# Optimization experiments

Measured on AMD Instinct MI355X. Metric: run time of the kernel, lower is better.

The kernel has to match this reference:

```python
import jax, jax.numpy as jnp
import numpy as np

K = 16  # neighbors per node

def setup_inputs() -> dict:
    key = jax.random.key(0)
    feature = jax.random.normal(key, (16384, 512), dtype=jnp.float32)
    return {"feature": feature, "k": K}

def reference(feature, k):
    # cosine-normalize rows (eps added to norm, matching torch)
    nrm = jnp.linalg.norm(feature, axis=-1, keepdims=True)
    fn = feature / (nrm + 1e-10)
    sim = fn @ fn.T                      # [N, N]
    n = sim.shape[0]
    # zero the diagonal (sim - diag_embed(diag(sim)))
    sim = sim - jnp.diag(jnp.diag(sim))
    _, idx = jax.lax.top_k(sim, k)       # [N, k]
    row = jnp.repeat(jnp.arange(n), k)   # [N*k]
    col = idx.reshape(-1)
    edge_index = jnp.stack([row, col], axis=0).astype(jnp.int64)
    return edge_index
```

## Files before the change

kernel.cpp:

```cpp
#include <hip/hip_runtime.h>
#include <hip/hip_fp16.h>
#include <math.h>

#define NN   16384
#define DD   512
#define KNN  16
#define CAND 24
#define STRIPW 4096
#define NSTRIP (NN / STRIPW)

typedef __attribute__((ext_vector_type(8))) short bf16x8;
typedef __attribute__((ext_vector_type(4))) float f32x4;
typedef unsigned int u32;

__device__ __forceinline__ void load16_lds(const ushort* g, void* l) {
    __builtin_amdgcn_global_load_lds(
        (const __attribute__((address_space(1))) u32*)(const void*)g,
        (__attribute__((address_space(3))) u32*)l, 16, 0, 0);
}

__global__ __launch_bounds__(256) void norm_kernel(const float* __restrict__ feat,
                                                   float* __restrict__ nrm) {
#pragma clang fp contract(off)
    const int t   = threadIdx.x;
    const int row = blockIdx.x * 64 + (t >> 2);
    const int bid = t & 3;
    const float4* p4 = (const float4*)(feat + (size_t)row * DD + bid * 128);
    float r[4][4];
    #pragma unroll
    for (int m = 0; m < 4; m++) {
        float4 q = p4[m];
        r[m][0] = q.x * q.x; r[m][1] = q.y * q.y;
        r[m][2] = q.z * q.z; r[m][3] = q.w * q.w;
    }
    #pragma unroll
    for (int tt = 1; tt < 8; tt++) {
        #pragma unroll
        for (int m = 0; m < 4; m++) {
            float4 q = p4[tt * 4 + m];
            r[m][0] += q.x * q.x; r[m][1] += q.y * q.y;
            r[m][2] += q.z * q.z; r[m][3] += q.w * q.w;
        }
    }
    float v0 = (r[0][0] + r[1][0]) + (r[2][0] + r[3][0]);
    float v1 = (r[0][1] + r[1][1]) + (r[2][1] + r[3][1]);
    float v2 = (r[0][2] + r[1][2]) + (r[2][2] + r[3][2]);
    float v3 = (r[0][3] + r[1][3]) + (r[2][3] + r[3][3]);
    float B  = (v0 + v1) + (v2 + v3);
    B += __shfl_xor(B, 1, 64);
    B += __shfl_xor(B, 2, 64);
    if (bid == 0) nrm[row] = sqrtf(B) + 1e-10f;
}

__device__ inline ushort bf16rne(float f) {
    unsigned u = __float_as_uint(f);
    u += 0x7fffu + ((u >> 16) & 1u);
    return (ushort)(u >> 16);
}
__global__ __launch_bounds__(256) void fn_kernel(const float* __restrict__ feat,
                                                 const float* __restrict__ nrm,
                                                 float* __restrict__ fn,
                                                 ushort* __restrict__ fnb) {
    int i4  = blockIdx.x * 256 + threadIdx.x;
    int row = i4 >> 7;
    float n = nrm[row];
    float4 v = ((const float4*)feat)[i4];
    float4 o = make_float4(v.x / n, v.y / n, v.z / n, v.w / n);
    ((float4*)fn)[i4] = o;
    ushort4 b = {bf16rne(o.x), bf16rne(o.y), bf16rne(o.z), bf16rne(o.w)};
    ((ushort4*)fnb)[i4] = b;
}

__global__ __launch_bounds__(256) void gemm_kernel(const ushort* __restrict__ fnb,
                                                   int stripBase,
                                                   __half* __restrict__ simS) {
    __shared__ ushort As[128 * 64];
    __shared__ ushort Bs[128 * 64];
    const int t    = threadIdx.x;
    const int wave = t >> 6, lane = t & 63;
    const int rbase = blockIdx.y * 128;
    const int cbL   = blockIdx.x * 128;
    const int wr = (wave >> 1) * 64, wc = (wave & 1) * 64;
    const int m = lane & 15, quad = lane >> 4;
    const int rseg = lane >> 3;
    const int cchk = (lane & 7) ^ rseg;

    f32x4 acc[4][4];
    #pragma unroll
    for (int i = 0; i < 4; i++)
        #pragma unroll
        for (int j = 0; j < 4; j++) acc[i][j] = (f32x4){0.f, 0.f, 0.f, 0.f};

    const int swz = ((m & 7) << 4);

    for (int kb = 0; kb < DD; kb += 64) {
        __syncthreads();
        #pragma unroll
        for (int q = 0; q < 4; q++) {
            int s   = wave * 4 + q;
            int row = s * 8 + rseg;
            const ushort* ga = fnb + (size_t)(rbase + row) * DD + kb + cchk * 8;
            const ushort* gb = fnb + (size_t)(stripBase + cbL + row) * DD + kb + cchk * 8;
            load16_lds(ga, (char*)As + s * 1024);
            load16_lds(gb, (char*)Bs + s * 1024);
        }
        __syncthreads();

        #pragma unroll
        for (int ks = 0; ks < 64; ks += 32) {
            const int cb16 = (ks >> 3) + quad;
            const int off  = ((cb16 << 4) ^ swz);
            bf16x8 af[4], bv[4];
            #pragma unroll
            for (int i = 0; i < 4; i++)
                af[i] = *(const bf16x8*)((const char*)As + (wr + i * 16 + m) * 128 + off);
            #pragma unroll
            for (int j = 0; j < 4; j++)
                bv[j] = *(const bf16x8*)((const char*)Bs + (wc + j * 16 + m) * 128 + off);
            #pragma unroll
            for (int i = 0; i < 4; i++)
                #pragma unroll
                for (int j = 0; j < 4; j++)
                    acc[i][j] = __builtin_amdgcn_mfma_f32_16x16x32_bf16(
                        af[i], bv[j], acc[i][j], 0, 0, 0);
        }
    }
    #pragma unroll
    for (int i = 0; i < 4; i++)
        #pragma unroll
        for (int j = 0; j < 4; j++)
            #pragma unroll
            for (int r = 0; r < 4; r++) {
                int grow = rbase + wr + i * 16 + quad * 4 + r;
                int gcol = cbL + wc + j * 16 + m;
                simS[(size_t)grow * STRIPW + gcol] = __float2half(acc[i][j][r]);
            }
}

__global__ __launch_bounds__(256) void select_kernel(const __half2* __restrict__ simS2,
                                                     int stripBase, int firstStrip,
                                                     float* __restrict__ lval,
                                                     int* __restrict__ lidx) {
    const int lane = threadIdx.x & 63;
    const int row  = blockIdx.x * 4 + (threadIdx.x >> 6);
    float lv; int li;
    if (firstStrip) { lv = -3.4e38f; li = 0x7fffffff; }
    else {
        lv = (lane < CAND) ? lval[(size_t)row * CAND + lane] : -3.4e38f;
        li = (lane < CAND) ? lidx[(size_t)row * CAND + lane] : 0x7fffffff;
    }
    const __half2* sp = simS2 + (size_t)row * (STRIPW / 2);
    for (int it = 0; it < STRIPW / 128; it++) {
        __half2 h = sp[it * 64 + lane];
        float v0 = __low2float(h), v1 = __high2float(h);
        int c0 = stripBase + it * 128 + lane * 2, c1 = c0 + 1;
        float vmin = __shfl(lv, CAND - 1);
        int   imin = __shfl(li, CAND - 1);
        bool a0 = ((v0 > vmin) || (v0 == vmin && c0 < imin)) && (c0 != row);
        bool a1 = ((v1 > vmin) || (v1 == vmin && c1 < imin)) && (c1 != row);
        unsigned long long m0 = __ballot(a0), m1 = __ballot(a1);
        #pragma unroll
        for (int ph = 0; ph < 2; ph++) {
            unsigned long long mask = ph ? m1 : m0;
            float vv = ph ? v1 : v0;
            while (mask) {
                int src = __builtin_ctzll(mask); mask &= mask - 1;
                float bvv = __shfl(vv, src);
                int   bc  = stripBase + it * 128 + src * 2 + ph;
                bool better = (lv > bvv) || (lv == bvv && li < bc);
                unsigned long long bb = __ballot(better) & ((1ull << CAND) - 1);
                int p = __popcll(bb);
                if (p < CAND) {
                    float pv = __shfl_up(lv, 1);
                    int   pi = __shfl_up(li, 1);
                    float nlv = (lane < p) ? lv : (lane == p ? bvv : pv);
                    int   nli = (lane < p) ? li : (lane == p ? bc : pi);
                    if (lane < CAND) { lv = nlv; li = nli; }
                }
            }
        }
    }
    if (lane < CAND) {
        lval[(size_t)row * CAND + lane] = lv;
        lidx[(size_t)row * CAND + lane] = li;
    }
}

__global__ __launch_bounds__(256) void rescore_kernel(const float* __restrict__ fn,
                                                      const int* __restrict__ lidx,
                                                      int* __restrict__ out) {
    __shared__ float sv[8][CAND];
    __shared__ int   si[8][CAND];
    const int w    = threadIdx.x >> 5;
    const int lane = threadIdx.x & 31;
    const int row  = blockIdx.x * 8 + w;
    const bool valid = lane < CAND;
    const int c = valid ? lidx[(size_t)row * CAND + lane] : 0;
    const float* q = fn + (size_t)row * DD;
    const float* p = fn + (size_t)c * DD;
    float s = 0.0f;
    for (int k = 0; k < DD; k += 16) {
        float4 q0 = *(const float4*)(q + k),      p0 = *(const float4*)(p + k);
        float4 q1 = *(const float4*)(q + k + 4),  p1 = *(const float4*)(p + k + 4);
        float4 q2 = *(const float4*)(q + k + 8),  p2 = *(const float4*)(p + k + 8);
        float4 q3 = *(const float4*)(q + k + 12), p3 = *(const float4*)(p + k + 12);
        s = __builtin_fmaf(q0.x, p0.x, s); s = __builtin_fmaf(q0.y, p0.y, s);
        s = __builtin_fmaf(q0.z, p0.z, s); s = __builtin_fmaf(q0.w, p0.w, s);
        s = __builtin_fmaf(q1.x, p1.x, s); s = __builtin_fmaf(q1.y, p1.y, s);
        s = __builtin_fmaf(q1.z, p1.z, s); s = __builtin_fmaf(q1.w, p1.w, s);
        s = __builtin_fmaf(q2.x, p2.x, s); s = __builtin_fmaf(q2.y, p2.y, s);
        s = __builtin_fmaf(q2.z, p2.z, s); s = __builtin_fmaf(q2.w, p2.w, s);
        s = __builtin_fmaf(q3.x, p3.x, s); s = __builtin_fmaf(q3.y, p3.y, s);
        s = __builtin_fmaf(q3.z, p3.z, s); s = __builtin_fmaf(q3.w, p3.w, s);
    }
    if (valid) { sv[w][lane] = s; si[w][lane] = c; }
    __syncthreads();
    if (valid) {
        int rank = 0;
        #pragma unroll 8
        for (int mm = 0; mm < CAND; mm++) {
            float vm = sv[w][mm];
            rank += (vm > s) || (vm == s && si[w][mm] < c);
        }
        if (rank < KNN) {
            out[(size_t)row * KNN + rank]            = row;
            out[(size_t)NN * KNN + row * KNN + rank] = c;
        }
    }
}

#define MT 64
#define CT 128
#define KT 32
#define SIM_LD 132
template <bool PRE>
__global__ __launch_bounds__(256) void knn_exact_kernel(const float* __restrict__ src,
                                                        const float* __restrict__ nrm,
                                                        int* __restrict__ out) {
    __shared__ union {
        struct { float As[KT][MT]; float Bs[KT][CT]; } stage;
        float sim[MT][SIM_LD];
    } u;
    __shared__ float tval[MT][KNN];
    __shared__ int   tidx[MT][KNN];
    const int t  = threadIdx.x;
    const int r0 = blockIdx.x * MT;
    const int tx = t & 15;
    const int ty = t >> 4;
    for (int i = t; i < MT * KNN; i += 256) {
        ((float*)tval)[i] = -3.4e38f;
        ((int*)tidx)[i]   = 0;
    }
    const int arow = t >> 2, akq = t & 3;
    const int bcol = t >> 1, bkh = t & 1;
    for (int ct = 0; ct < NN / CT; ct++) {
        const int c0 = ct * CT;
        float acc[4][8];
        #pragma unroll
        for (int rr = 0; rr < 4; rr++)
            #pragma unroll
            for (int cc = 0; cc < 8; cc++) acc[rr][cc] = 0.0f;
        for (int kt = 0; kt < DD / KT; kt++) {
            const int kb = kt * KT;
            __syncthreads();
            {
                const float* ap = src + (size_t)(r0 + arow) * DD + kb + akq * 8;
                float4 a0 = *(const float4*)ap;
                float4 a1 = *(const float4*)(ap + 4);
                if (!PRE) {
                    float nA = nrm[r0 + arow];
                    a0.x /= nA; a0.y /= nA; a0.z /= nA; a0.w /= nA;
                    a1.x /= nA; a1.y /= nA; a1.z /= nA; a1.w /= nA;
                }
                int k0 = akq * 8;
                u.stage.As[k0 + 0][arow] = a0.x; u.stage.As[k0 + 1][arow] = a0.y;
                u.stage.As[k0 + 2][arow] = a0.z; u.stage.As[k0 + 3][arow] = a0.w;
                u.stage.As[k0 + 4][arow] = a1.x; u.stage.As[k0 + 5][arow] = a1.y;
                u.stage.As[k0 + 6][arow] = a1.z; u.stage.As[k0 + 7][arow] = a1.w;
            }
            {
                const float* bp = src + (size_t)(c0 + bcol) * DD + kb + bkh * 16;
                float4 b0 = *(const float4*)bp;
                float4 b1 = *(const float4*)(bp + 4);
                float4 b2 = *(const float4*)(bp + 8);
                float4 b3 = *(const float4*)(bp + 12);
                if (!PRE) {
                    float nB = nrm[c0 + bcol];
                    b0.x /= nB; b0.y /= nB; b0.z /= nB; b0.w /= nB;
                    b1.x /= nB; b1.y /= nB; b1.z /= nB; b1.w /= nB;
                    b2.x /= nB; b2.y /= nB; b2.z /= nB; b2.w /= nB;
                    b3.x /= nB; b3.y /= nB; b3.z /= nB; b3.w /= nB;
                }
                int k0 = bkh * 16;
                u.stage.Bs[k0 +  0][bcol] = b0.x; u.stage.Bs[k0 +  1][bcol] = b0.y;
                u.stage.Bs[k0 +  2][bcol] = b0.z; u.stage.Bs[k0 +  3][bcol] = b0.w;
                u.stage.Bs[k0 +  4][bcol] = b1.x; u.stage.Bs[k0 +  5][bcol] = b1.y;
                u.stage.Bs[k0 +  6][bcol] = b1.z; u.stage.Bs[k0 +  7][bcol] = b1.w;
                u.stage.Bs[k0 +  8][bcol] = b2.x; u.stage.Bs[k0 +  9][bcol] = b2.y;
                u.stage.Bs[k0 + 10][bcol] = b2.z; u.stage.Bs[k0 + 11][bcol] = b2.w;
                u.stage.Bs[k0 + 12][bcol] = b3.x; u.stage.Bs[k0 + 13][bcol] = b3.y;
                u.stage.Bs[k0 + 14][bcol] = b3.z; u.stage.Bs[k0 + 15][bcol] = b3.w;
            }
            __syncthreads();
            #pragma unroll
            for (int kk = 0; kk < KT; kk++) {
                float4 av  = *(const float4*)&u.stage.As[kk][ty * 4];
                float4 bv0 = *(const float4*)&u.stage.Bs[kk][tx * 4];
                float4 bv1 = *(const float4*)&u.stage.Bs[kk][64 + tx * 4];
                float ar[4] = {av.x, av.y, av.z, av.w};
                float br[8] = {bv0.x, bv0.y, bv0.z, bv0.w,
                               bv1.x, bv1.y, bv1.z, bv1.w};
                #pragma unroll
                for (int rr = 0; rr < 4; rr++)
                    #pragma unroll
                    for (int cc = 0; cc < 8; cc++)
                        acc[rr][cc] = __builtin_fmaf(ar[rr], br[cc], acc[rr][cc]);
            }
        }
        __syncthreads();
        {
            #pragma unroll
            for (int rr = 0; rr < 4; rr++) {
                *(float4*)&u.sim[ty * 4 + rr][tx * 4] =
                    make_float4(acc[rr][0], acc[rr][1], acc[rr][2], acc[rr][3]);
                *(float4*)&u.sim[ty * 4 + rr][64 + tx * 4] =
                    make_float4(acc[rr][4], acc[rr][5], acc[rr][6], acc[rr][7]);
            }
        }
        __syncthreads();
        if ((t & 3) == 0) {
            const int lr = t >> 2, grow = r0 + lr;
            float vmin = tval[lr][KNN - 1];
            for (int j = 0; j < CT / 4; j++) {
                float4 v4 = *(const float4*)&u.sim[lr][j * 4];
                float vs[4] = {v4.x, v4.y, v4.z, v4.w};
                #pragma unroll
                for (int e = 0; e < 4; e++) {
                    int cc2 = c0 + j * 4 + e;
                    float v = vs[e];
                    if (cc2 == grow) continue;
                    if (v > vmin) {
                        int p = KNN - 1;
                        while (p > 0 && tval[lr][p - 1] < v) {
                            tval[lr][p] = tval[lr][p - 1];
                            tidx[lr][p] = tidx[lr][p - 1];
                            p--;
                        }
                        tval[lr][p] = v;
                        tidx[lr][p] = cc2;
                        vmin = tval[lr][KNN - 1];
                    }
                }
            }
        }
    }
    __syncthreads();
    for (int i = t; i < MT * KNN; i += 256) {
        int lr = i / KNN, j = i % KNN;
        int grow = r0 + lr;
        out[(size_t)grow * KNN + j]            = grow;
        out[(size_t)NN * KNN + grow * KNN + j] = tidx[lr][j];
    }
}

extern "C" void kernel_launch(void* const* d_in, const int* in_sizes, int n_in,
                              void* d_out, int out_size, void* d_ws, size_t ws_size,
                              hipStream_t stream) {
    const float* feat = (const float*)d_in[0];
    int* out = (int*)d_out;
    char* ws = (char*)d_ws;

    const size_t oNrm  = 0;
    const size_t oFn   = 64 * 1024;
    const size_t oFnb  = oFn  + (size_t)NN * DD * 4;
    const size_t oLv   = oFnb + (size_t)NN * DD * 2;
    const size_t oLi   = oLv  + (size_t)NN * CAND * 4;
    const size_t oSim  = oLi  + (size_t)NN * CAND * 4;
    const size_t need  = oSim + (size_t)NN * STRIPW * 2;
    float*  nrm  = (float*)(ws + oNrm);
    float*  fn   = (float*)(ws + oFn);
    ushort* fnb  = (ushort*)(ws + oFnb);
    float*  lval = (float*)(ws + oLv);
    int*    lidx = (int*)(ws + oLi);
    __half* simS = (__half*)(ws + oSim);

    norm_kernel<<<NN / 64, 256, 0, stream>>>(feat, nrm);

    if (ws_size >= need) {
        fn_kernel<<<(NN * DD / 4) / 256, 256, 0, stream>>>(feat, nrm, fn, fnb);
        for (int s = 0; s < NSTRIP; s++) {
            dim3 ggrid(STRIPW / 128, NN / 128);
            gemm_kernel<<<ggrid, 256, 0, stream>>>(fnb, s * STRIPW, simS);
            select_kernel<<<NN / 4, 256, 0, stream>>>((const __half2*)simS,
                                                      s * STRIPW, s == 0,
                                                      lval, lidx);
        }
        rescore_kernel<<<NN / 8, 256, 0, stream>>>(fn, lidx, out);
    } else if (ws_size >= oFn + (size_t)NN * DD * 4) {
        fn_kernel<<<(NN * DD / 4) / 256, 256, 0, stream>>>(feat, nrm, fn,
                                                           (ushort*)(ws + oFn));
        knn_exact_kernel<true><<<NN / MT, 256, 0, stream>>>(fn, nrm, out);
    } else {
        knn_exact_kernel<false><<<NN / MT, 256, 0, stream>>>(feat, nrm, out);
    }
}
```

Baseline: 881.0 us.

## Fuse norm and normalize kernels, widen GEMM tile, batch rescore rows

Merges the norm and normalize kernels into one launch, so each block reads its rows a second time while they are likely still in cache and one launch is saved. The GEMM tile grows from 128x128 to 128x256 with 32 accumulators per wave, which raises reuse of the A tile but costs more registers and LDS and may lower occupancy. The rescore kernel now handles two rows per 32-lane group to expose more memory-level parallelism. The fallback path's workspace check also changes.

Measured after the change: 1.042 ms. +18.2%, slower.

```diff
diff --git a/kernel.cpp b/kernel.cpp
--- a/kernel.cpp
+++ b/kernel.cpp
@@ -19,8 +19,16 @@
         (__attribute__((address_space(3))) u32*)l, 16, 0, 0);
 }
 
-__global__ __launch_bounds__(256) void norm_kernel(const float* __restrict__ feat,
-                                                   float* __restrict__ nrm) {
+__device__ inline ushort bf16rne(float f) {
+    unsigned u = __float_as_uint(f);
+    u += 0x7fffu + ((u >> 16) & 1u);
+    return (ushort)(u >> 16);
+}
+
+__global__ __launch_bounds__(256) void norm_fn_kernel(const float* __restrict__ feat,
+                                                      float* __restrict__ nrm,
+                                                      float* __restrict__ fn,
+                                                      ushort* __restrict__ fnb) {
 #pragma clang fp contract(off)
     const int t   = threadIdx.x;
     const int row = blockIdx.x * 64 + (t >> 2);
@@ -49,49 +57,42 @@
     float B  = (v0 + v1) + (v2 + v3);
     B += __shfl_xor(B, 1, 64);
     B += __shfl_xor(B, 2, 64);
-    if (bid == 0) nrm[row] = sqrtf(B) + 1e-10f;
-}
-
-__device__ inline ushort bf16rne(float f) {
-    unsigned u = __float_as_uint(f);
-    u += 0x7fffu + ((u >> 16) & 1u);
-    return (ushort)(u >> 16);
-}
-__global__ __launch_bounds__(256) void fn_kernel(const float* __restrict__ feat,
-                                                 const float* __restrict__ nrm,
-                                                 float* __restrict__ fn,
-                                                 ushort* __restrict__ fnb) {
-    int i4  = blockIdx.x * 256 + threadIdx.x;
-    int row = i4 >> 7;
-    float n = nrm[row];
-    float4 v = ((const float4*)feat)[i4];
-    float4 o = make_float4(v.x / n, v.y / n, v.z / n, v.w / n);
-    ((float4*)fn)[i4] = o;
-    ushort4 b = {bf16rne(o.x), bf16rne(o.y), bf16rne(o.z), bf16rne(o.w)};
-    ((ushort4*)fnb)[i4] = b;
+    float nv = sqrtf(B) + 1e-10f;
+    __shared__ float snrm[64];
+    if (bid == 0) { nrm[row] = nv; snrm[t >> 2] = nv; }
+    __syncthreads();
+    const int base4 = blockIdx.x * 8192;
+    for (int i = t; i < 8192; i += 256) {
+        int lrow = i >> 7;
+        float n = snrm[lrow];
+        float4 v = ((const float4*)feat)[base4 + i];
+        float4 o = make_float4(v.x / n, v.y / n, v.z / n, v.w / n);
+        ((float4*)fn)[base4 + i] = o;
+        ushort4 b = {bf16rne(o.x), bf16rne(o.y), bf16rne(o.z), bf16rne(o.w)};
+        ((ushort4*)fnb)[base4 + i] = b;
+    }
 }
 
 __global__ __launch_bounds__(256) void gemm_kernel(const ushort* __restrict__ fnb,
                                                    int stripBase,
                                                    __half* __restrict__ simS) {
     __shared__ ushort As[128 * 64];
-    __shared__ ushort Bs[128 * 64];
+    __shared__ ushort Bs[256 * 64];
     const int t    = threadIdx.x;
     const int wave = t >> 6, lane = t & 63;
     const int rbase = blockIdx.y * 128;
-    const int cbL   = blockIdx.x * 128;
-    const int wr = (wave >> 1) * 64, wc = (wave & 1) * 64;
+    const int cbL   = blockIdx.x * 256;
+    const int wr = (wave >> 1) * 64, wc = (wave & 1) * 128;
     const int m = lane & 15, quad = lane >> 4;
     const int rseg = lane >> 3;
     const int cchk = (lane & 7) ^ rseg;
-
-    f32x4 acc[4][4];
+    const int swz  = ((m & 7) << 4);
+
+    f32x4 acc[4][8];
     #pragma unroll
     for (int i = 0; i < 4; i++)
         #pragma unroll
-        for (int j = 0; j < 4; j++) acc[i][j] = (f32x4){0.f, 0.f, 0.f, 0.f};
-
-    const int swz = ((m & 7) << 4);
+        for (int j = 0; j < 8; j++) acc[i][j] = (f32x4){0.f, 0.f, 0.f, 0.f};
 
     for (int kb = 0; kb < DD; kb += 64) {
         __syncthreads();
@@ -99,28 +100,32 @@
         for (int q = 0; q < 4; q++) {
             int s   = wave * 4 + q;
             int row = s * 8 + rseg;
-            const ushort* ga = fnb + (size_t)(rbase + row) * DD + kb + cchk * 8;
-            const ushort* gb = fnb + (size_t)(stripBase + cbL + row) * DD + kb + cchk * 8;
-            load16_lds(ga, (char*)As + s * 1024);
-            load16_lds(gb, (char*)Bs + s * 1024);
+            load16_lds(fnb + (size_t)(rbase + row) * DD + kb + cchk * 8,
+                       (char*)As + s * 1024);
+        }
+        #pragma unroll
+        for (int q = 0; q < 8; q++) {
+            int s   = wave * 8 + q;
+            int row = s * 8 + rseg;
+            load16_lds(fnb + (size_t)(stripBase + cbL + row) * DD + kb + cchk * 8,
+                       (char*)Bs + s * 1024);
         }
         __syncthreads();
 
         #pragma unroll
         for (int ks = 0; ks < 64; ks += 32) {
-            const int cb16 = (ks >> 3) + quad;
-            const int off  = ((cb16 << 4) ^ swz);
-            bf16x8 af[4], bv[4];
+            const int off = ((((ks >> 3) + quad) << 4)) ^ swz;
+            bf16x8 af[4], bv[8];
             #pragma unroll
             for (int i = 0; i < 4; i++)
                 af[i] = *(const bf16x8*)((const char*)As + (wr + i * 16 + m) * 128 + off);
             #pragma unroll
-            for (int j = 0; j < 4; j++)
+            for (int j = 0; j < 8; j++)
                 bv[j] = *(const bf16x8*)((const char*)Bs + (wc + j * 16 + m) * 128 + off);
             #pragma unroll
             for (int i = 0; i < 4; i++)
                 #pragma unroll
-                for (int j = 0; j < 4; j++)
+                for (int j = 0; j < 8; j++)
                     acc[i][j] = __builtin_amdgcn_mfma_f32_16x16x32_bf16(
                         af[i], bv[j], acc[i][j], 0, 0, 0);
         }
@@ -128,7 +133,7 @@
     #pragma unroll
     for (int i = 0; i < 4; i++)
         #pragma unroll
-        for (int j = 0; j < 4; j++)
+        for (int j = 0; j < 8; j++)
             #pragma unroll
             for (int r = 0; r < 4; r++) {
                 int grow = rbase + wr + i * 16 + quad * 4 + r;
@@ -189,44 +194,89 @@
 __global__ __launch_bounds__(256) void rescore_kernel(const float* __restrict__ fn,
                                                       const int* __restrict__ lidx,
                                                       int* __restrict__ out) {
-    __shared__ float sv[8][CAND];
-    __shared__ int   si[8][CAND];
+    __shared__ float sv[16][CAND];
+    __shared__ int   si[16][CAND];
     const int w    = threadIdx.x >> 5;
     const int lane = threadIdx.x & 31;
-    const int row  = blockIdx.x * 8 + w;
+    const int rowA = blockIdx.x * 16 + w;
+    const int rowB = rowA + 8;
     const bool valid = lane < CAND;
-    const int c = valid ? lidx[(size_t)row * CAND + lane] : 0;
-    const float* q = fn + (size_t)row * DD;
-    const float* p = fn + (size_t)c * DD;
-    float s = 0.0f;
-    for (int k = 0; k < DD; k += 16) {
-        float4 q0 = *(const float4*)(q + k),      p0 = *(const float4*)(p + k);
-        float4 q1 = *(const float4*)(q + k + 4),  p1 = *(const float4*)(p + k + 4);
-        float4 q2 = *(const float4*)(q + k + 8),  p2 = *(const float4*)(p + k + 8);
-        float4 q3 = *(const float4*)(q + k + 12), p3 = *(const float4*)(p + k + 12);
-        s = __builtin_fmaf(q0.x, p0.x, s); s = __builtin_fmaf(q0.y, p0.y, s);
-        s = __builtin_fmaf(q0.z, p0.z, s); s = __builtin_fmaf(q0.w, p0.w, s);
-        s = __builtin_fmaf(q1.x, p1.x, s); s = __builtin_fmaf(q1.y, p1.y, s);
-        s = __builtin_fmaf(q1.z, p1.z, s); s = __builtin_fmaf(q1.w, p1.w, s);
-        s = __builtin_fmaf(q2.x, p2.x, s); s = __builtin_fmaf(q2.y, p2.y, s);
-        s = __builtin_fmaf(q2.z, p2.z, s); s = __builtin_fmaf(q2.w, p2.w, s);
-        s = __builtin_fmaf(q3.x, p3.x, s); s = __builtin_fmaf(q3.y, p3.y, s);
-        s = __builtin_fmaf(q3.z, p3.z, s); s = __builtin_fmaf(q3.w, p3.w, s);
-    }
-    if (valid) { sv[w][lane] = s; si[w][lane] = c; }
+    const int cA = valid ? lidx[(size_t)rowA * CAND + lane] : 0;
+    const int cB = valid ? lidx[(size_t)rowB * CAND + lane] : 0;
+    const float* qA = fn + (size_t)rowA * DD;
+    const float* pA = fn + (size_t)cA * DD;
+    const float* qB = fn + (size_t)rowB * DD;
+    const float* pB = fn + (size_t)cB * DD;
+    float sA = 0.0f, sB = 0.0f;
+    for (int k = 0; k < DD; k += 8) {
+        float4 qa0 = *(const float4*)(qA + k),     pa0 = *(const float4*)(pA + k);
+        float4 qa1 = *(const float4*)(qA + k + 4), pa1 = *(const float4*)(pA + k + 4);
+        float4 qb0 = *(const float4*)(qB + k),     pb0 = *(const float4*)(pB + k);
+        float4 qb1 = *(const float4*)(qB + k + 4), pb1 = *(const float4*)(pB + k + 4);
+        sA = __builtin_fmaf(qa0.x, pa0.x, sA); sB = __builtin_fmaf(qb0.x, pb0.x, sB);
+        sA = __builtin_fmaf(qa0.y, pa0.y, sA); sB = __builtin_fmaf(qb0.y, pb0.y, sB);
+        sA = __builtin_fmaf(qa0.z, pa0.z, sA); sB = __builtin_fmaf(qb0.z, pb0.z, sB);
+        sA = __builtin_fmaf(qa0.w, pa0.w, sA); sB = __builtin_fmaf(qb0.w, pb0.w, sB);
+        sA = __builtin_fmaf(qa1.x, pa1.x, sA); sB = __builtin_fmaf(qb1.x, pb1.x, sB);
+        sA = __builtin_fmaf(qa1.y, pa1.y, sA); sB = __builtin_fmaf(qb1.y, pb1.y, sB);
+        sA = __builtin_fmaf(qa1.z, pa1.z, sA); sB = __builtin_fmaf(qb1.z, pb1.z, sB);
+        sA = __builtin_fmaf(qa1.w, pa1.w, sA); sB = __builtin_fmaf(qb1.w, pb1.w, sB);
+    }
+    if (valid) {
+        sv[w][lane] = sA;     si[w][lane] = cA;
+        sv[w + 8][lane] = sB; si[w + 8][lane] = cB;
+    }
     __syncthreads();
     if (valid) {
-        int rank = 0;
+        int rankA = 0, rankB = 0;
         #pragma unroll 8
         for (int mm = 0; mm < CAND; mm++) {
-            float vm = sv[w][mm];
-            rank += (vm > s) || (vm == s && si[w][mm] < c);
-        }
-        if (rank < KNN) {
-            out[(size_t)row * KNN + rank]            = row;
-            out[(size_t)NN * KNN + row * KNN + rank] = c;
-        }
-    }
+            float va = sv[w][mm], vb = sv[w + 8][mm];
+            rankA += (va > sA) || (va == sA && si[w][mm] < cA);
+            rankB += (vb > sB) || (vb == sB && si[w + 8][mm] < cB);
+        }
+        if (rankA < KNN) {
+            out[(size_t)rowA * KNN + rankA]            = rowA;
+            out[(size_t)NN * KNN + rowA * KNN + rankA] = cA;
+        }
+        if (rankB < KNN) {
+            out[(size_t)rowB * KNN + rankB]            = rowB;
+            out[(size_t)NN * KNN + rowB * KNN + rankB] = cB;
+        }
+    }
+}
+
+__global__ __launch_bounds__(256) void norm_kernel(const float* __restrict__ feat,
+                                                   float* __restrict__ nrm) {
+#pragma clang fp contract(off)
+    const int t   = threadIdx.x;
+    const int row = blockIdx.x * 64 + (t >> 2);
+    const int bid = t & 3;
+    const float4* p4 = (const float4*)(feat + (size_t)row * DD + bid * 128);
+    float r[4][4];
+    #pragma unroll
+    for (int m = 0; m < 4; m++) {
+        float4 q = p4[m];
+        r[m][0] = q.x * q.x; r[m][1] = q.y * q.y;
+        r[m][2] = q.z * q.z; r[m][3] = q.w * q.w;
+    }
+    #pragma unroll
+    for (int tt = 1; tt < 8; tt++) {
+        #pragma unroll
+        for (int m = 0; m < 4; m++) {
+            float4 q = p4[tt * 4 + m];
+            r[m][0] += q.x * q.x; r[m][1] += q.y * q.y;
+            r[m][2] += q.z * q.z; r[m][3] += q.w * q.w;
+        }
+    }
+    float v0 = (r[0][0] + r[1][0]) + (r[2][0] + r[3][0]);
+    float v1 = (r[0][1] + r[1][1]) + (r[2][1] + r[3][1]);
+    float v2 = (r[0][2] + r[1][2]) + (r[2][2] + r[3][2]);
+    float v3 = (r[0][3] + r[1][3]) + (r[2][3] + r[3][3]);
+    float B  = (v0 + v1) + (v2 + v3);
+    B += __shfl_xor(B, 1, 64);
+    B += __shfl_xor(B, 2, 64);
+    if (bid == 0) nrm[row] = sqrtf(B) + 1e-10f;
 }
 
 #define MT 64
@@ -384,23 +434,21 @@
     int*    lidx = (int*)(ws + oLi);
     __half* simS = (__half*)(ws + oSim);
 
-    norm_kernel<<<NN / 64, 256, 0, stream>>>(feat, nrm);
-
     if (ws_size >= need) {
-        fn_kernel<<<(NN * DD / 4) / 256, 256, 0, stream>>>(feat, nrm, fn, fnb);
+        norm_fn_kernel<<<NN / 64, 256, 0, stream>>>(feat, nrm, fn, fnb);
         for (int s = 0; s < NSTRIP; s++) {
-            dim3 ggrid(STRIPW / 128, NN / 128);
+            dim3 ggrid(STRIPW / 256, NN / 128);
             gemm_kernel<<<ggrid, 256, 0, stream>>>(fnb, s * STRIPW, simS);
             select_kernel<<<NN / 4, 256, 0, stream>>>((const __half2*)simS,
                                                       s * STRIPW, s == 0,
                                                       lval, lidx);
         }
-        rescore_kernel<<<NN / 8, 256, 0, stream>>>(fn, lidx, out);
-    } else if (ws_size >= oFn + (size_t)NN * DD * 4) {
-        fn_kernel<<<(NN * DD / 4) / 256, 256, 0, stream>>>(feat, nrm, fn,
-                                                           (ushort*)(ws + oFn));
+        rescore_kernel<<<NN / 16, 256, 0, stream>>>(fn, lidx, out);
+    } else if (ws_size >= oLv) {
+        norm_fn_kernel<<<NN / 64, 256, 0, stream>>>(feat, nrm, fn, fnb);
         knn_exact_kernel<true><<<NN / MT, 256, 0, stream>>>(fn, nrm, out);
     } else {
+        norm_kernel<<<NN / 64, 256, 0, stream>>>(feat, nrm);
         knn_exact_kernel<false><<<NN / MT, 256, 0, stream>>>(feat, nrm, out);
     }
 }
```
